# Kernel optimization log

Hardware: AMD Instinct MI355X
Metric: run time of the kernel (lower is better)

The kernel has to match this reference:

```python
import jax, jax.numpy as jnp
import numpy as np
from jax import lax

B = 1024
D_VQ = 64
KS = 1024
KX = 1024
BETA = 0.25


def _conv1d(x, w, b):
    # x: [N, Cin, L], w: [Cout, Cin, 3], 'same' padding
    y = lax.conv_general_dilated(x, w, (1,), [(1, 1)], dimension_numbers=('NCH', 'OIH', 'NCH'))
    return y + b[None, :, None]


def _conv2d(x, w, b):
    # x: [N, Cin, H, W], w: [Cout, Cin, 3, 3], 'same' padding
    y = lax.conv_general_dilated(x, w, (1, 1), [(1, 1), (1, 1)], dimension_numbers=('NCHW', 'OIHW', 'NCHW'))
    return y + b[None, :, None, None]


def _gelu(x):
    return jax.nn.gelu(x, approximate=False)


def _vq_ema(z_e, codebook, beta):
    # z_e: [N, D], codebook: [K, D]
    d = (jnp.sum(z_e * z_e, axis=1, keepdims=True)
         - 2.0 * (z_e @ codebook.T)
         + jnp.sum(codebook * codebook, axis=1)[None, :])  # [N, K]
    idx = jnp.argmin(d, axis=1)                              # [N]
    z_q = codebook[idx]                                      # gather [N, D]
    vq_loss = beta * jnp.mean((z_e - lax.stop_gradient(z_q)) ** 2)
    z_q_st = z_e + lax.stop_gradient(z_q - z_e)              # straight-through
    n = z_e.shape[0]
    probs = jnp.zeros((codebook.shape[0],), z_e.dtype).at[idx].add(1.0) / n
    perplexity = jnp.exp(-jnp.sum(probs * jnp.log(probs + 1e-10)))
    return z_q_st, idx, vq_loss, perplexity


def setup_inputs() -> dict:
    key = jax.random.key(0)
    ks = iter(jax.random.split(key, 40))

    def p(shape, s=0.05):
        return jax.random.normal(next(ks), shape, jnp.float32) * s

    inp = {
        'cubes': jax.random.normal(next(ks), (B, 9, 8, 72), jnp.float32),
        # spectral encoder
        's_w1': p((16, 1, 3)), 's_b1': jnp.zeros((16,), jnp.float32),
        's_w2': p((16, 16, 3)), 's_b2': jnp.zeros((16,), jnp.float32),
        's_fc_w': p((D_VQ, 16 * 8)), 's_fc_b': jnp.zeros((D_VQ,), jnp.float32),
        'cb_s': p((KS, D_VQ), 1.0),
        # spectral decoder
        's_dec_fc_w': p((16 * 8, D_VQ)), 's_dec_fc_b': jnp.zeros((16 * 8,), jnp.float32),
        's_dec_w1': p((16, 16, 3)), 's_dec_b1': jnp.zeros((16,), jnp.float32),
        's_dec_w2': p((1, 16, 3)), 's_dec_b2': jnp.zeros((1,), jnp.float32),
        # spatial encoder
        'x_w1': p((16, 8, 3, 3)), 'x_b1': jnp.zeros((16,), jnp.float32),
        'x_w2': p((16, 16, 3, 3)), 'x_b2': jnp.zeros((16,), jnp.float32),
        'x_fc_w': p((D_VQ, 16 * 3 * 3)), 'x_fc_b': jnp.zeros((D_VQ,), jnp.float32),
        'cb_x': p((KX, D_VQ), 1.0),
        # spatial decoder
        'x_dec_fc_w': p((16 * 3 * 3, D_VQ)), 'x_dec_fc_b': jnp.zeros((16 * 3 * 3,), jnp.float32),
        'x_dec_w1': p((16, 16, 3, 3)), 'x_dec_b1': jnp.zeros((16,), jnp.float32),
        'x_dec_w2': p((8, 16, 3, 3)), 'x_dec_b2': jnp.zeros((8,), jnp.float32),
        'return_recon': 1,
    }
    return inp


def reference(cubes, s_w1, s_b1, s_w2, s_b2, s_fc_w, s_fc_b, cb_s,
              s_dec_fc_w, s_dec_fc_b, s_dec_w1, s_dec_b1, s_dec_w2, s_dec_b2,
              x_w1, x_b1, x_w2, x_b2, x_fc_w, x_fc_b, cb_x,
              x_dec_fc_w, x_dec_fc_b, x_dec_w1, x_dec_b1, x_dec_w2, x_dec_b2,
              return_recon):
    b, p, t, f = cubes.shape
    n = b * p * t
    c6 = cubes.reshape(b, p, t, 8, 3, 3)                   # [B,P,T,8,3,3]
    cperm = jnp.transpose(c6, (0, 1, 2, 4, 5, 3))          # [B,P,T,3,3,8]

    # --- spectral path ---
    spec = jnp.mean(cperm, axis=(3, 4))                    # [B,P,T,8]
    spec_seq = spec.reshape(n, 1, 8)
    s = _gelu(_conv1d(spec_seq, s_w1, s_b1))
    s = _gelu(_conv1d(s, s_w2, s_b2))
    z_e_s = s.reshape(n, 16 * 8) @ s_fc_w.T + s_fc_b       # [N,D]
    z_q_s, k_idx, vq_loss_s, perplex_s = _vq_ema(z_e_s, cb_s, BETA)
    emb_s = z_q_s.reshape(b, p, t, D_VQ)
    k_idx = k_idx.reshape(b, p, t)

    # --- spatial path ---
    spatial = c6.reshape(n, 8, 3, 3)
    x = _gelu(_conv2d(spatial, x_w1, x_b1))
    x = _gelu(_conv2d(x, x_w2, x_b2))
    z_e_x = x.reshape(n, 16 * 9) @ x_fc_w.T + x_fc_b
    z_q_x, m_idx, vq_loss_x, perplex_x = _vq_ema(z_e_x, cb_x, BETA)
    emb_x = z_q_x.reshape(b, p, t, D_VQ)
    m_idx = m_idx.reshape(b, p, t)

    total = vq_loss_s + vq_loss_x

    if return_recon:
        s_dec = (z_q_s @ s_dec_fc_w.T + s_dec_fc_b).reshape(n, 16, 8)
        s_dec = _gelu(_conv1d(s_dec, s_dec_w1, s_dec_b1))
        recon_s = _conv1d(s_dec, s_dec_w2, s_dec_b2)[:, 0, :].reshape(b, p, t, 8)
        recon_loss_s = jnp.mean((recon_s - spec) ** 2)

        x_dec = (z_q_x @ x_dec_fc_w.T + x_dec_fc_b).reshape(n, 16, 3, 3)
        x_dec = _gelu(_conv2d(x_dec, x_dec_w1, x_dec_b1))
        recon_x = _conv2d(x_dec, x_dec_w2, x_dec_b2)        # [N,8,3,3]
        recon_loss_x = jnp.mean((recon_x - spatial) ** 2)
        recon_loss_total = recon_loss_s + recon_loss_x
    else:
        recon_loss_total = jnp.float32(0.0)

    return (emb_s, emb_x, k_idx, m_idx, total, perplex_s, perplex_x, recon_loss_total)
```

## Files before the change

kernel.cpp:

```cpp
#include <hip/hip_runtime.h>
#include <math.h>

#define NTOK 73728

__device__ __forceinline__ float gelu_f(float x) {
    return 0.5f * x * (1.0f + erff(x * 0.70710678118654752440f));
}

__global__ void k_norms(const float* __restrict__ cb_s, const float* __restrict__ cb_x,
                        double* __restrict__ cn_s, double* __restrict__ cn_x) {
    int i = blockIdx.x * blockDim.x + threadIdx.x;
    if (i >= 2048) return;
    const float* cb = (i < 1024) ? cb_s : cb_x;
    double* cn = (i < 1024) ? cn_s : cn_x;
    int c = i & 1023;
    double s = 0.0;
    for (int k = 0; k < 64; ++k) { double v = (double)cb[c * 64 + k]; s += v * v; }
    cn[c] = s;
}

__global__ void k_transpose(const float* __restrict__ src, float* __restrict__ dst, int E) {
    int i = blockIdx.x * 256 + threadIdx.x;
    if (i >= 64 * E) return;
    int e = i >> 6, d = i & 63;
    dst[i] = src[d * E + e];
}

__global__ void k_weff_s(const float* __restrict__ w1, const float* __restrict__ b1,
                         const float* __restrict__ dfcw, const float* __restrict__ dfcb,
                         float* __restrict__ weffT, float* __restrict__ beff) {
    int idx = blockIdx.x * 256 + threadIdx.x;
    if (idx >= 128 * 64) return;
    int o = idx >> 6, d = idx & 63;
    int c = o >> 3, l = o & 7;
    double acc = 0.0;
    for (int ci = 0; ci < 16; ++ci)
        for (int dd = 0; dd < 3; ++dd) {
            int ll = l + dd - 1;
            if (ll < 0 || ll > 7) continue;
            acc += (double)w1[(c * 16 + ci) * 3 + dd] * (double)dfcw[(ci * 8 + ll) * 64 + d];
        }
    weffT[d * 132 + o] = (float)acc;
    if (o < 4) weffT[d * 132 + 128 + o] = 0.f;
    if (d == 0) {
        double bb = (double)b1[c];
        for (int ci = 0; ci < 16; ++ci)
            for (int dd = 0; dd < 3; ++dd) {
                int ll = l + dd - 1;
                if (ll < 0 || ll > 7) continue;
                bb += (double)w1[(c * 16 + ci) * 3 + dd] * (double)dfcb[ci * 8 + ll];
            }
        beff[o] = (float)bb;
    }
}

__global__ void k_weff_x(const float* __restrict__ w1, const float* __restrict__ b1,
                         const float* __restrict__ dfcw, const float* __restrict__ dfcb,
                         float* __restrict__ weffT, float* __restrict__ beff) {
    int idx = blockIdx.x * 256 + threadIdx.x;
    if (idx >= 144 * 64) return;
    int o = idx >> 6, d = idx & 63;
    int c = o / 9, p = o - c * 9;
    int i = p / 3, j = p % 3;
    double acc = 0.0;
    for (int ci = 0; ci < 16; ++ci)
        for (int di = 0; di < 3; ++di) {
            int ii = i + di - 1; if (ii < 0 || ii > 2) continue;
            for (int dj = 0; dj < 3; ++dj) {
                int jj = j + dj - 1; if (jj < 0 || jj > 2) continue;
                acc += (double)w1[((c * 16 + ci) * 3 + di) * 3 + dj]
                     * (double)dfcw[(ci * 9 + ii * 3 + jj) * 64 + d];
            }
        }
    weffT[d * 148 + o] = (float)acc;
    if (o < 4) weffT[d * 148 + 144 + o] = 0.f;
    if (d == 0) {
        double bb = (double)b1[c];
        for (int ci = 0; ci < 16; ++ci)
            for (int di = 0; di < 3; ++di) {
                int ii = i + di - 1; if (ii < 0 || ii > 2) continue;
                for (int dj = 0; dj < 3; ++dj) {
                    int jj = j + dj - 1; if (jj < 0 || jj > 2) continue;
                    bb += (double)w1[((c * 16 + ci) * 3 + di) * 3 + dj]
                        * (double)dfcb[ci * 9 + ii * 3 + jj];
                }
            }
        beff[o] = (float)bb;
    }
}

__global__ void __launch_bounds__(256) k_spec_enc(
    const float* __restrict__ cubes,
    const float* __restrict__ w1, const float* __restrict__ b1,
    const float* __restrict__ w2, const float* __restrict__ b2,
    const float* __restrict__ fcwT, const float* __restrict__ fcb,
    float* __restrict__ z_out)
{
    __shared__ float S[16 * 8];
    __shared__ float A[16 * 136];
    __shared__ float Bb[16 * 136];
    int tid = threadIdx.x;
    int t = tid >> 4, c = tid & 15;
    if (tid < 128) {
        int tk = tid >> 3, f = tid & 7;
        const float* cu = cubes + ((size_t)blockIdx.x * 16 + tk) * 72 + f * 9;
        float s = 0.f;
        #pragma unroll
        for (int k = 0; k < 9; ++k) s += cu[k];
        S[tk * 8 + f] = s * (1.0f / 9.0f);
    }
    __syncthreads();
    {
        float s0[8];
        *(float4*)&s0[0] = *(const float4*)&S[t * 8];
        *(float4*)&s0[4] = *(const float4*)&S[t * 8 + 4];
        float wa = w1[c * 3 + 0], wb = w1[c * 3 + 1], wc = w1[c * 3 + 2], bb = b1[c];
        #pragma unroll
        for (int l = 0; l < 8; ++l) {
            float v = fmaf(wb, s0[l], bb);
            if (l > 0) v = fmaf(wa, s0[l - 1], v);
            if (l < 7) v = fmaf(wc, s0[l + 1], v);
            A[t * 136 + c * 8 + l] = gelu_f(v);
        }
    }
    __syncthreads();
    {
        float acc[8];
        #pragma unroll
        for (int l = 0; l < 8; ++l) acc[l] = b2[c];
        for (int ci = 0; ci < 16; ++ci) {
            float r[8];
            *(float4*)&r[0] = *(const float4*)&A[t * 136 + ci * 8];
            *(float4*)&r[4] = *(const float4*)&A[t * 136 + ci * 8 + 4];
            float wa = w2[(c * 16 + ci) * 3 + 0], wb = w2[(c * 16 + ci) * 3 + 1], wc = w2[(c * 16 + ci) * 3 + 2];
            #pragma unroll
            for (int l = 0; l < 8; ++l) {
                if (l > 0) acc[l] = fmaf(wa, r[l - 1], acc[l]);
                acc[l] = fmaf(wb, r[l], acc[l]);
                if (l < 7) acc[l] = fmaf(wc, r[l + 1], acc[l]);
            }
        }
        #pragma unroll
        for (int l = 0; l < 8; ++l) Bb[t * 136 + c * 8 + l] = gelu_f(acc[l]);
    }
    __syncthreads();
    {
        float4 zv = make_float4(fcb[c * 4 + 0], fcb[c * 4 + 1], fcb[c * 4 + 2], fcb[c * 4 + 3]);
        #pragma unroll 4
        for (int e = 0; e < 128; ++e) {
            float be = Bb[t * 136 + e];
            float4 wv = *(const float4*)(fcwT + (e << 6) + (c << 2));
            zv.x = fmaf(wv.x, be, zv.x);
            zv.y = fmaf(wv.y, be, zv.y);
            zv.z = fmaf(wv.z, be, zv.z);
            zv.w = fmaf(wv.w, be, zv.w);
        }
        *(float4*)(z_out + ((size_t)blockIdx.x * 16 + t) * 64 + c * 4) = zv;
    }
}

__global__ void __launch_bounds__(256) k_spat_enc(
    const float* __restrict__ cubes,
    const float* __restrict__ w1, const float* __restrict__ b1,
    const float* __restrict__ w2, const float* __restrict__ b2,
    const float* __restrict__ fcwT, const float* __restrict__ fcb,
    float* __restrict__ z_out)
{
    __shared__ float A[16 * 200];
    __shared__ float Bb[16 * 200];
    int tid = threadIdx.x;
    int t = tid >> 4, c = tid & 15;
    for (int u = tid; u < 1152; u += 256) {
        int tk = u / 72, e = u - tk * 72;
        int ci = e / 9, p = e - ci * 9;
        A[tk * 200 + ci * 12 + p] = cubes[(size_t)blockIdx.x * 1152 + u];
    }
    __syncthreads();
    {
        float acc[9];
        #pragma unroll
        for (int p = 0; p < 9; ++p) acc[p] = b1[c];
        for (int ci = 0; ci < 8; ++ci) {
            float r[12];
            *(float4*)&r[0] = *(const float4*)&A[t * 200 + ci * 12];
            *(float4*)&r[4] = *(const float4*)&A[t * 200 + ci * 12 + 4];
            *(float4*)&r[8] = *(const float4*)&A[t * 200 + ci * 12 + 8];
            const float* w = w1 + (c * 8 + ci) * 9;
            #pragma unroll
            for (int p = 0; p < 9; ++p) {
                int i = p / 3, j = p % 3;
                #pragma unroll
                for (int di = 0; di < 3; ++di) {
                    int ii = i + di - 1; if (ii < 0 || ii > 2) continue;
                    #pragma unroll
                    for (int dj = 0; dj < 3; ++dj) {
                        int jj = j + dj - 1; if (jj < 0 || jj > 2) continue;
                        acc[p] = fmaf(w[di * 3 + dj], r[ii * 3 + jj], acc[p]);
                    }
                }
            }
        }
        #pragma unroll
        for (int p = 0; p < 9; ++p) Bb[t * 200 + c * 12 + p] = gelu_f(acc[p]);
    }
    __syncthreads();
    {
        float acc[9];
        #pragma unroll
        for (int p = 0; p < 9; ++p) acc[p] = b2[c];
        for (int ci = 0; ci < 16; ++ci) {
            float r[12];
            *(float4*)&r[0] = *(const float4*)&Bb[t * 200 + ci * 12];
            *(float4*)&r[4] = *(const float4*)&Bb[t * 200 + ci * 12 + 4];
            *(float4*)&r[8] = *(const float4*)&Bb[t * 200 + ci * 12 + 8];
            const float* w = w2 + (c * 16 + ci) * 9;
            #pragma unroll
            for (int p = 0; p < 9; ++p) {
                int i = p / 3, j = p % 3;
                #pragma unroll
                for (int di = 0; di < 3; ++di) {
                    int ii = i + di - 1; if (ii < 0 || ii > 2) continue;
                    #pragma unroll
                    for (int dj = 0; dj < 3; ++dj) {
                        int jj = j + dj - 1; if (jj < 0 || jj > 2) continue;
                        acc[p] = fmaf(w[di * 3 + dj], r[ii * 3 + jj], acc[p]);
                    }
                }
            }
        }
        __syncthreads();
        #pragma unroll
        for (int p = 0; p < 9; ++p) A[t * 200 + c * 12 + p] = gelu_f(acc[p]);
    }
    __syncthreads();
    {
        float4 zv = make_float4(fcb[c * 4 + 0], fcb[c * 4 + 1], fcb[c * 4 + 2], fcb[c * 4 + 3]);
        #pragma unroll 4
        for (int e = 0; e < 144; ++e) {
            int ci = e / 9, p = e - ci * 9;
            float be = A[t * 200 + ci * 12 + p];
            float4 wv = *(const float4*)(fcwT + (e << 6) + (c << 2));
            zv.x = fmaf(wv.x, be, zv.x);
            zv.y = fmaf(wv.y, be, zv.y);
            zv.z = fmaf(wv.z, be, zv.z);
            zv.w = fmaf(wv.w, be, zv.w);
        }
        *(float4*)(z_out + ((size_t)blockIdx.x * 16 + t) * 64 + c * 4) = zv;
    }
}

__global__ void __launch_bounds__(256) k_vq(
    float* __restrict__ emb, const float* __restrict__ cb,
    const double* __restrict__ cn,
    float* __restrict__ idx_out, int* __restrict__ hist,
    double* __restrict__ partial)
{
    __shared__ double pbest[4][64];
    __shared__ int pidx[4][64];
    __shared__ int lh[1024];
    int tid = threadIdx.x;
    int w = tid >> 6, l = tid & 63;
    for (int u = tid; u < 1024; u += 256) lh[u] = 0;
    size_t n = (size_t)blockIdx.x * 64 + l;
    float z[64];
    {
        const float4* zp = (const float4*)(emb + n * 64);
        #pragma unroll
        for (int k = 0; k < 16; ++k) *(float4*)&z[k * 4] = zp[k];
    }
    int base = __builtin_amdgcn_readfirstlane(w << 8);
    const float* crb = cb + ((size_t)base << 6);
    const double* cnb = cn + base;
    double best = 1e300; int bi = base;
    for (int cc = 0; cc < 256; ++cc) {
        const float* cr = crb + (cc << 6);
        float d0 = 0.f, d1 = 0.f, d2 = 0.f, d3 = 0.f;
        #pragma unroll
        for (int k = 0; k < 64; k += 4) {
            d0 = fmaf(z[k + 0], cr[k + 0], d0);
            d1 = fmaf(z[k + 1], cr[k + 1], d1);
            d2 = fmaf(z[k + 2], cr[k + 2], d2);
            d3 = fmaf(z[k + 3], cr[k + 3], d3);
        }
        float dot = (d0 + d1) + (d2 + d3);
        double dd = cnb[cc] - 2.0 * (double)dot;
        if (dd < best) { best = dd; bi = base + cc; }
    }
    pbest[w][l] = best; pidx[w][l] = bi;
    __syncthreads();
    if (w == 0) {
        double b = pbest[0][l]; int bj = pidx[0][l];
        #pragma unroll
        for (int q = 1; q < 4; ++q) {
            double d = pbest[q][l];
            if (d < b) { b = d; bj = pidx[q][l]; }
        }
        idx_out[n] = (float)bj;
        float qv[64];
        {
            const float4* cq = (const float4*)(cb + ((size_t)bj << 6));
            #pragma unroll
            for (int k = 0; k < 16; ++k) *(float4*)&qv[k * 4] = cq[k];
        }
        float vs = 0.f;
        #pragma unroll
        for (int k = 0; k < 64; ++k) { float df = z[k] - qv[k]; vs = fmaf(df, df, vs); }
        float4* zo = (float4*)(emb + n * 64);
        #pragma unroll
        for (int k = 0; k < 16; ++k) zo[k] = *(float4*)&qv[k * 4];
        atomicAdd(&lh[bj], 1);
        double s = (double)vs;
        #pragma unroll
        for (int o = 32; o > 0; o >>= 1) s += __shfl_down(s, o);
        if (l == 0) partial[blockIdx.x] = s;
    }
    __syncthreads();
    for (int u = tid; u < 1024; u += 256) if (lh[u] > 0) atomicAdd(&hist[u], lh[u]);
}

__global__ void __launch_bounds__(256) k_spec_dec(
    const float* __restrict__ emb, const float* __restrict__ cubes,
    const float* __restrict__ weffT, const float* __restrict__ beff,
    const float* __restrict__ w2, const float* __restrict__ b2,
    double* __restrict__ partial)
{
    __shared__ float Z[16 * 72];
    __shared__ float Bb[16 * 136];
    __shared__ float S[16 * 8];
    __shared__ double wred[4];
    int tid = threadIdx.x;
    int t = tid >> 4, c = tid & 15;
    {
        int tk = tid >> 4, dq = tid & 15;
        *(float4*)&Z[tk * 72 + dq * 4] =
            *(const float4*)(emb + (size_t)blockIdx.x * 1024 + (size_t)tid * 4);
    }
    if (tid < 128) {
        int tk = tid >> 3, f = tid & 7;
        const float* cu = cubes + ((size_t)blockIdx.x * 16 + tk) * 72 + f * 9;
        float s = 0.f;
        #pragma unroll
        for (int k = 0; k < 9; ++k) s += cu[k];
        S[tk * 8 + f] = s * (1.0f / 9.0f);
    }
    __syncthreads();
    float zr[64];
    #pragma unroll
    for (int k = 0; k < 16; ++k) *(float4*)&zr[k * 4] = *(const float4*)&Z[t * 72 + k * 4];
    {
        float4 a0 = make_float4(0.f, 0.f, 0.f, 0.f);
        float4 a1 = make_float4(0.f, 0.f, 0.f, 0.f);
        #pragma unroll 8
        for (int k = 0; k < 64; ++k) {
            float zk = zr[k];
            float4 w0 = *(const float4*)(weffT + k * 132 + (c << 2));
            float4 w1v = *(const float4*)(weffT + k * 132 + 64 + (c << 2));
            a0.x = fmaf(w0.x, zk, a0.x); a0.y = fmaf(w0.y, zk, a0.y);
            a0.z = fmaf(w0.z, zk, a0.z); a0.w = fmaf(w0.w, zk, a0.w);
            a1.x = fmaf(w1v.x, zk, a1.x); a1.y = fmaf(w1v.y, zk, a1.y);
            a1.z = fmaf(w1v.z, zk, a1.z); a1.w = fmaf(w1v.w, zk, a1.w);
        }
        int o0 = c << 2, o1 = 64 + (c << 2);
        float4 g0 = make_float4(gelu_f(a0.x + beff[o0 + 0]), gelu_f(a0.y + beff[o0 + 1]),
                                gelu_f(a0.z + beff[o0 + 2]), gelu_f(a0.w + beff[o0 + 3]));
        float4 g1 = make_float4(gelu_f(a1.x + beff[o1 + 0]), gelu_f(a1.y + beff[o1 + 1]),
                                gelu_f(a1.z + beff[o1 + 2]), gelu_f(a1.w + beff[o1 + 3]));
        *(float4*)&Bb[t * 136 + o0] = g0;
        *(float4*)&Bb[t * 136 + o1] = g1;
    }
    __syncthreads();
    float acc2 = 0.f;
    {
        int h = c >> 3, pos = c & 7;
        float a = (h == 0) ? b2[0] : 0.f;
        for (int ci = h * 8; ci < h * 8 + 8; ++ci) {
            const float* w = w2 + ci * 3;
            const float* hb = &Bb[t * 136 + ci * 8];
            if (pos > 0) a = fmaf(w[0], hb[pos - 1], a);
            a = fmaf(w[1], hb[pos], a);
            if (pos < 7) a = fmaf(w[2], hb[pos + 1], a);
        }
        a += __shfl_xor(a, 8);
        if (h == 0) { float df = a - S[t * 8 + pos]; acc2 = df * df; }
    }
    double s = (double)acc2;
    #pragma unroll
    for (int o = 32; o > 0; o >>= 1) s += __shfl_down(s, o);
    if ((tid & 63) == 0) wred[tid >> 6] = s;
    __syncthreads();
    if (tid == 0) partial[blockIdx.x] = wred[0] + wred[1] + wred[2] + wred[3];
}

__global__ void __launch_bounds__(256) k_spat_dec(
    const float* __restrict__ emb, const float* __restrict__ cubes,
    const float* __restrict__ weffT, const float* __restrict__ beff,
    const float* __restrict__ w2, const float* __restrict__ b2,
    double* __restrict__ partial)
{
    __shared__ float Z[16 * 72];
    __shared__ float H[16 * 200];
    __shared__ float T[16 * 104];
    __shared__ double wred[4];
    int tid = threadIdx.x;
    int t = tid >> 4, c = tid & 15;
    {
        int tk = tid >> 4, dq = tid & 15;
        *(float4*)&Z[tk * 72 + dq * 4] =
            *(const float4*)(emb + (size_t)blockIdx.x * 1024 + (size_t)tid * 4);
    }
    for (int u = tid; u < 1152; u += 256) {
        int tk = u / 72, e = u - tk * 72;
        int ci = e / 9, p = e - ci * 9;
        T[tk * 104 + ci * 12 + p] = cubes[(size_t)blockIdx.x * 1152 + u];
    }
    __syncthreads();
    float zr[64];
    #pragma unroll
    for (int k = 0; k < 16; ++k) *(float4*)&zr[k * 4] = *(const float4*)&Z[t * 72 + k * 4];
    {
        float4 a0 = make_float4(0.f, 0.f, 0.f, 0.f);
        float4 a1 = make_float4(0.f, 0.f, 0.f, 0.f);
        float4 a2 = make_float4(0.f, 0.f, 0.f, 0.f);
        #pragma unroll 8
        for (int k = 0; k < 64; ++k) {
            float zk = zr[k];
            float4 w0 = *(const float4*)(weffT + k * 148 + (c << 2));
            float4 w1v = *(const float4*)(weffT + k * 148 + 64 + (c << 2));
            float4 w2v = *(const float4*)(weffT + k * 148 + 128 + (c << 2));
            a0.x = fmaf(w0.x, zk, a0.x); a0.y = fmaf(w0.y, zk, a0.y);
            a0.z = fmaf(w0.z, zk, a0.z); a0.w = fmaf(w0.w, zk, a0.w);
            a1.x = fmaf(w1v.x, zk, a1.x); a1.y = fmaf(w1v.y, zk, a1.y);
            a1.z = fmaf(w1v.z, zk, a1.z); a1.w = fmaf(w1v.w, zk, a1.w);
            a2.x = fmaf(w2v.x, zk, a2.x); a2.y = fmaf(w2v.y, zk, a2.y);
            a2.z = fmaf(w2v.z, zk, a2.z); a2.w = fmaf(w2v.w, zk, a2.w);
        }
        float av[12] = {a0.x, a0.y, a0.z, a0.w, a1.x, a1.y, a1.z, a1.w, a2.x, a2.y, a2.z, a2.w};
        #pragma unroll
        for (int q = 0; q < 12; ++q) {
            int o = (c << 2) + ((q >> 2) << 6) + (q & 3);
            int ch = o / 9, p = o - ch * 9;
            H[t * 200 + ch * 12 + p] = gelu_f(av[q] + beff[o]);
        }
    }
    __syncthreads();
    float acc2 = 0.f;
    {
        int co = c >> 1, h = c & 1;
        float accp[9];
        #pragma unroll
        for (int p = 0; p < 9; ++p) accp[p] = (h == 0) ? b2[co] : 0.f;
        for (int ci = h * 8; ci < h * 8 + 8; ++ci) {
            float r[12];
            *(float4*)&r[0] = *(const float4*)&H[t * 200 + ci * 12];
            *(float4*)&r[4] = *(const float4*)&H[t * 200 + ci * 12 + 4];
            *(float4*)&r[8] = *(const float4*)&H[t * 200 + ci * 12 + 8];
            const float* w = w2 + (co * 16 + ci) * 9;
            #pragma unroll
            for (int p = 0; p < 9; ++p) {
                int i = p / 3, j = p % 3;
                #pragma unroll
                for (int di = 0; di < 3; ++di) {
                    int ii = i + di - 1; if (ii < 0 || ii > 2) continue;
                    #pragma unroll
                    for (int dj = 0; dj < 3; ++dj) {
                        int jj = j + dj - 1; if (jj < 0 || jj > 2) continue;
                        accp[p] = fmaf(w[di * 3 + dj], r[ii * 3 + jj], accp[p]);
                    }
                }
            }
        }
        #pragma unroll
        for (int p = 0; p < 9; ++p) {
            float tot = accp[p] + __shfl_xor(accp[p], 1);
            if (h == 0) { float df = tot - T[t * 104 + co * 12 + p]; acc2 = fmaf(df, df, acc2); }
        }
    }
    double s = (double)acc2;
    #pragma unroll
    for (int o = 32; o > 0; o >>= 1) s += __shfl_down(s, o);
    if ((tid & 63) == 0) wred[tid >> 6] = s;
    __syncthreads();
    if (tid == 0) partial[blockIdx.x] = wred[0] + wred[1] + wred[2] + wred[3];
}

__global__ void __launch_bounds__(256) k_final(
    const double* __restrict__ p_vq_s, const double* __restrict__ p_vq_x,
    const double* __restrict__ p_rec_s, const double* __restrict__ p_rec_x,
    const int* __restrict__ hist_s, const int* __restrict__ hist_x,
    const int* __restrict__ rr,
    float* __restrict__ outscal)
{
    __shared__ double wred[4];
    int tid = threadIdx.x;
    auto bred = [&](double v) -> double {
        #pragma unroll
        for (int o = 32; o > 0; o >>= 1) v += __shfl_down(v, o);
        __syncthreads();
        if ((tid & 63) == 0) wred[tid >> 6] = v;
        __syncthreads();
        return wred[0] + wred[1] + wred[2] + wred[3];
    };
    double a;
    a = 0; for (int t = tid; t < 1152; t += 256) a += p_vq_s[t];
    double vq_s = bred(a);
    a = 0; for (int t = tid; t < 1152; t += 256) a += p_vq_x[t];
    double vq_x = bred(a);
    a = 0; for (int t = tid; t < 4608; t += 256) a += p_rec_s[t];
    double rec_s = bred(a);
    a = 0; for (int t = tid; t < 4608; t += 256) a += p_rec_x[t];
    double rec_x = bred(a);
    a = 0;
    for (int t = tid; t < 1024; t += 256) {
        double cnt = (double)hist_s[t];
        if (cnt > 0.0) { double p = cnt / (double)NTOK; a += p * log(p + 1e-10); }
    }
    double ent_s = bred(a);
    a = 0;
    for (int t = tid; t < 1024; t += 256) {
        double cnt = (double)hist_x[t];
        if (cnt > 0.0) { double p = cnt / (double)NTOK; a += p * log(p + 1e-10); }
    }
    double ent_x = bred(a);
    if (tid == 0) {
        double total = 0.25 * (vq_s / 4718592.0 + vq_x / 4718592.0);
        double rec = (rr[0] != 0) ? (rec_s / 589824.0 + rec_x / 5308416.0) : 0.0;
        outscal[0] = (float)total;
        outscal[1] = (float)exp(-ent_s);
        outscal[2] = (float)exp(-ent_x);
        outscal[3] = (float)rec;
    }
}

extern "C" void kernel_launch(void* const* d_in, const int* in_sizes, int n_in,
                              void* d_out, int out_size, void* d_ws, size_t ws_size,
                              hipStream_t stream)
{
    const float* cubes  = (const float*)d_in[0];
    const float* s_w1   = (const float*)d_in[1];
    const float* s_b1   = (const float*)d_in[2];
    const float* s_w2   = (const float*)d_in[3];
    const float* s_b2   = (const float*)d_in[4];
    const float* s_fcw  = (const float*)d_in[5];
    const float* s_fcb  = (const float*)d_in[6];
    const float* cb_s   = (const float*)d_in[7];
    const float* s_dfcw = (const float*)d_in[8];
    const float* s_dfcb = (const float*)d_in[9];
    const float* s_dw1  = (const float*)d_in[10];
    const float* s_db1  = (const float*)d_in[11];
    const float* s_dw2  = (const float*)d_in[12];
    const float* s_db2  = (const float*)d_in[13];
    const float* x_w1   = (const float*)d_in[14];
    const float* x_b1   = (const float*)d_in[15];
    const float* x_w2   = (const float*)d_in[16];
    const float* x_b2   = (const float*)d_in[17];
    const float* x_fcw  = (const float*)d_in[18];
    const float* x_fcb  = (const float*)d_in[19];
    const float* cb_x   = (const float*)d_in[20];
    const float* x_dfcw = (const float*)d_in[21];
    const float* x_dfcb = (const float*)d_in[22];
    const float* x_dw1  = (const float*)d_in[23];
    const float* x_db1  = (const float*)d_in[24];
    const float* x_dw2  = (const float*)d_in[25];
    const float* x_db2  = (const float*)d_in[26];
    const int*   rr     = (const int*)d_in[27];

    float* out   = (float*)d_out;
    float* emb_s = out;
    float* emb_x = out + 4718592;
    float* kidx  = out + 9437184;
    float* midx  = out + 9510912;
    float* scal  = out + 9584640;

    char* ws = (char*)d_ws;
    int*    hist_s  = (int*)(ws + 0);
    int*    hist_x  = (int*)(ws + 4096);
    double* cn_s    = (double*)(ws + 8192);
    double* cn_x    = (double*)(ws + 16384);
    double* p_vq_s  = (double*)(ws + 24576);
    double* p_vq_x  = (double*)(ws + 33792);
    double* p_rec_s = (double*)(ws + 43008);
    double* p_rec_x = (double*)(ws + 79872);
    float*  beff_s  = (float*)(ws + 116736);
    float*  beff_x  = (float*)(ws + 117248);
    float*  weffT_s = (float*)(ws + 117888);
    float*  weffT_x = (float*)(ws + 151680);
    float*  fcwT_s  = (float*)(ws + 189568);
    float*  fcwT_x  = (float*)(ws + 222336);

    hipMemsetAsync(d_ws, 0, 8192, stream);
    k_norms<<<16, 128, 0, stream>>>(cb_s, cb_x, cn_s, cn_x);
    k_weff_s<<<32, 256, 0, stream>>>(s_dw1, s_db1, s_dfcw, s_dfcb, weffT_s, beff_s);
    k_weff_x<<<36, 256, 0, stream>>>(x_dw1, x_db1, x_dfcw, x_dfcb, weffT_x, beff_x);
    k_transpose<<<32, 256, 0, stream>>>(s_fcw, fcwT_s, 128);
    k_transpose<<<36, 256, 0, stream>>>(x_fcw, fcwT_x, 144);
    k_spec_enc<<<4608, 256, 0, stream>>>(cubes, s_w1, s_b1, s_w2, s_b2, fcwT_s, s_fcb, emb_s);
    k_spat_enc<<<4608, 256, 0, stream>>>(cubes, x_w1, x_b1, x_w2, x_b2, fcwT_x, x_fcb, emb_x);
    k_vq<<<1152, 256, 0, stream>>>(emb_s, cb_s, cn_s, kidx, hist_s, p_vq_s);
    k_vq<<<1152, 256, 0, stream>>>(emb_x, cb_x, cn_x, midx, hist_x, p_vq_x);
    k_spec_dec<<<4608, 256, 0, stream>>>(emb_s, cubes, weffT_s, beff_s, s_dw2, s_db2, p_rec_s);
    k_spat_dec<<<4608, 256, 0, stream>>>(emb_x, cubes, weffT_x, beff_x, x_dw2, x_db2, p_rec_x);
    k_final<<<1, 256, 0, stream>>>(p_vq_s, p_vq_x, p_rec_s, p_rec_x, hist_s, hist_x, rr, scal);
}
```

Before: 1.078 ms.

## Merge prep kernels, transpose conv weights, stage VQ codebook tiles in LDS

Combines the five small preprocessing launches into one k_prep kernel. The same kernel also writes channel-minor transposed copies of the conv weights, so the encoder and decoder conv loops make coalesced weight loads. The VQ kernel now stages 32-row codebook tiles per wave in shared memory with float4 reads, instead of each lane reading rows from global memory. It also drops the per-block LDS histogram in favour of direct global atomics, which may add atomic contention on popular codes.

```diff
diff --git a/kernel.cpp b/kernel.cpp
--- a/kernel.cpp
+++ b/kernel.cpp
@@ -7,92 +7,119 @@
     return 0.5f * x * (1.0f + erff(x * 0.70710678118654752440f));
 }
 
-__global__ void k_norms(const float* __restrict__ cb_s, const float* __restrict__ cb_x,
-                        double* __restrict__ cn_s, double* __restrict__ cn_x) {
-    int i = blockIdx.x * blockDim.x + threadIdx.x;
-    if (i >= 2048) return;
-    const float* cb = (i < 1024) ? cb_s : cb_x;
-    double* cn = (i < 1024) ? cn_s : cn_x;
-    int c = i & 1023;
-    double s = 0.0;
-    for (int k = 0; k < 64; ++k) { double v = (double)cb[c * 64 + k]; s += v * v; }
-    cn[c] = s;
-}
-
-__global__ void k_transpose(const float* __restrict__ src, float* __restrict__ dst, int E) {
-    int i = blockIdx.x * 256 + threadIdx.x;
-    if (i >= 64 * E) return;
-    int e = i >> 6, d = i & 63;
-    dst[i] = src[d * E + e];
-}
-
-__global__ void k_weff_s(const float* __restrict__ w1, const float* __restrict__ b1,
-                         const float* __restrict__ dfcw, const float* __restrict__ dfcb,
-                         float* __restrict__ weffT, float* __restrict__ beff) {
-    int idx = blockIdx.x * 256 + threadIdx.x;
-    if (idx >= 128 * 64) return;
-    int o = idx >> 6, d = idx & 63;
-    int c = o >> 3, l = o & 7;
-    double acc = 0.0;
-    for (int ci = 0; ci < 16; ++ci)
-        for (int dd = 0; dd < 3; ++dd) {
-            int ll = l + dd - 1;
-            if (ll < 0 || ll > 7) continue;
-            acc += (double)w1[(c * 16 + ci) * 3 + dd] * (double)dfcw[(ci * 8 + ll) * 64 + d];
-        }
-    weffT[d * 132 + o] = (float)acc;
-    if (o < 4) weffT[d * 132 + 128 + o] = 0.f;
-    if (d == 0) {
-        double bb = (double)b1[c];
+__global__ void __launch_bounds__(256) k_prep(
+    const float* __restrict__ cb_s, const float* __restrict__ cb_x,
+    double* __restrict__ cn_s, double* __restrict__ cn_x,
+    const float* __restrict__ s_dw1, const float* __restrict__ s_db1,
+    const float* __restrict__ s_dfcw, const float* __restrict__ s_dfcb,
+    float* __restrict__ weffT_s, float* __restrict__ beff_s,
+    const float* __restrict__ x_dw1, const float* __restrict__ x_db1,
+    const float* __restrict__ x_dfcw, const float* __restrict__ x_dfcb,
+    float* __restrict__ weffT_x, float* __restrict__ beff_x,
+    const float* __restrict__ s_fcw, float* __restrict__ fcwT_s,
+    const float* __restrict__ x_fcw, float* __restrict__ fcwT_x,
+    const float* __restrict__ s_w2, float* __restrict__ sw2T,
+    const float* __restrict__ x_w1, float* __restrict__ xw1T,
+    const float* __restrict__ x_w2, float* __restrict__ xw2T,
+    const float* __restrict__ x_dw2, float* __restrict__ xdw2T)
+{
+    int bid = blockIdx.x, tid = threadIdx.x;
+    if (bid < 8) {
+        int i = bid * 256 + tid;
+        const float* cb = (i < 1024) ? cb_s : cb_x;
+        double* cn = (i < 1024) ? cn_s : cn_x;
+        int c = i & 1023;
+        double s = 0.0;
+        for (int k = 0; k < 64; ++k) { double v = (double)cb[c * 64 + k]; s += v * v; }
+        cn[c] = s;
+    } else if (bid < 40) {
+        int idx = (bid - 8) * 256 + tid;
+        int o = idx >> 6, d = idx & 63;
+        int c = o >> 3, l = o & 7;
+        double acc = 0.0;
         for (int ci = 0; ci < 16; ++ci)
             for (int dd = 0; dd < 3; ++dd) {
                 int ll = l + dd - 1;
                 if (ll < 0 || ll > 7) continue;
-                bb += (double)w1[(c * 16 + ci) * 3 + dd] * (double)dfcb[ci * 8 + ll];
+                acc += (double)s_dw1[(c * 16 + ci) * 3 + dd] * (double)s_dfcw[(ci * 8 + ll) * 64 + d];
             }
-        beff[o] = (float)bb;
-    }
-}
-
-__global__ void k_weff_x(const float* __restrict__ w1, const float* __restrict__ b1,
-                         const float* __restrict__ dfcw, const float* __restrict__ dfcb,
-                         float* __restrict__ weffT, float* __restrict__ beff) {
-    int idx = blockIdx.x * 256 + threadIdx.x;
-    if (idx >= 144 * 64) return;
-    int o = idx >> 6, d = idx & 63;
-    int c = o / 9, p = o - c * 9;
-    int i = p / 3, j = p % 3;
-    double acc = 0.0;
-    for (int ci = 0; ci < 16; ++ci)
-        for (int di = 0; di < 3; ++di) {
-            int ii = i + di - 1; if (ii < 0 || ii > 2) continue;
-            for (int dj = 0; dj < 3; ++dj) {
-                int jj = j + dj - 1; if (jj < 0 || jj > 2) continue;
-                acc += (double)w1[((c * 16 + ci) * 3 + di) * 3 + dj]
-                     * (double)dfcw[(ci * 9 + ii * 3 + jj) * 64 + d];
-            }
-        }
-    weffT[d * 148 + o] = (float)acc;
-    if (o < 4) weffT[d * 148 + 144 + o] = 0.f;
-    if (d == 0) {
-        double bb = (double)b1[c];
+        weffT_s[d * 132 + o] = (float)acc;
+        if (o < 4) weffT_s[d * 132 + 128 + o] = 0.f;
+        if (d == 0) {
+            double bb = (double)s_db1[c];
+            for (int ci = 0; ci < 16; ++ci)
+                for (int dd = 0; dd < 3; ++dd) {
+                    int ll = l + dd - 1;
+                    if (ll < 0 || ll > 7) continue;
+                    bb += (double)s_dw1[(c * 16 + ci) * 3 + dd] * (double)s_dfcb[ci * 8 + ll];
+                }
+            beff_s[o] = (float)bb;
+        }
+    } else if (bid < 76) {
+        int idx = (bid - 40) * 256 + tid;
+        int o = idx >> 6, d = idx & 63;
+        int c = o / 9, p = o - c * 9;
+        int i = p / 3, j = p % 3;
+        double acc = 0.0;
         for (int ci = 0; ci < 16; ++ci)
             for (int di = 0; di < 3; ++di) {
                 int ii = i + di - 1; if (ii < 0 || ii > 2) continue;
                 for (int dj = 0; dj < 3; ++dj) {
                     int jj = j + dj - 1; if (jj < 0 || jj > 2) continue;
-                    bb += (double)w1[((c * 16 + ci) * 3 + di) * 3 + dj]
-                        * (double)dfcb[ci * 9 + ii * 3 + jj];
+                    acc += (double)x_dw1[((c * 16 + ci) * 3 + di) * 3 + dj]
+                         * (double)x_dfcw[(ci * 9 + ii * 3 + jj) * 64 + d];
                 }
             }
-        beff[o] = (float)bb;
+        weffT_x[d * 148 + o] = (float)acc;
+        if (o < 4) weffT_x[d * 148 + 144 + o] = 0.f;
+        if (d == 0) {
+            double bb = (double)x_db1[c];
+            for (int ci = 0; ci < 16; ++ci)
+                for (int di = 0; di < 3; ++di) {
+                    int ii = i + di - 1; if (ii < 0 || ii > 2) continue;
+                    for (int dj = 0; dj < 3; ++dj) {
+                        int jj = j + dj - 1; if (jj < 0 || jj > 2) continue;
+                        bb += (double)x_dw1[((c * 16 + ci) * 3 + di) * 3 + dj]
+                            * (double)x_dfcb[ci * 9 + ii * 3 + jj];
+                    }
+                }
+            beff_x[o] = (float)bb;
+        }
+    } else if (bid < 108) {
+        int i = (bid - 76) * 256 + tid;
+        fcwT_s[i] = s_fcw[(i & 63) * 128 + (i >> 6)];
+    } else if (bid < 144) {
+        int i = (bid - 108) * 256 + tid;
+        fcwT_x[i] = x_fcw[(i & 63) * 144 + (i >> 6)];
+    } else {
+        int i = (bid - 144) * 256 + tid;
+        if (i < 768) {
+            int c = i & 15, r = i >> 4;
+            int ci = r / 3, dd = r % 3;
+            sw2T[i] = s_w2[(c * 16 + ci) * 3 + dd];
+        } else if (i < 1920) {
+            int j = i - 768;
+            int c = j & 15, r = j >> 4;
+            int ci = r / 9, tap = r % 9;
+            xw1T[j] = x_w1[(c * 8 + ci) * 9 + tap];
+        } else if (i < 4224) {
+            int j = i - 1920;
+            int c = j & 15, r = j >> 4;
+            int ci = r / 9, tap = r % 9;
+            xw2T[j] = x_w2[(c * 16 + ci) * 9 + tap];
+        } else {
+            int j = i - 4224;
+            int co = j & 7, r = j >> 3;
+            int ci = r / 9, tap = r % 9;
+            xdw2T[j] = x_dw2[(co * 16 + ci) * 9 + tap];
+        }
     }
 }
 
 __global__ void __launch_bounds__(256) k_spec_enc(
     const float* __restrict__ cubes,
     const float* __restrict__ w1, const float* __restrict__ b1,
-    const float* __restrict__ w2, const float* __restrict__ b2,
+    const float* __restrict__ sw2T, const float* __restrict__ b2,
     const float* __restrict__ fcwT, const float* __restrict__ fcb,
     float* __restrict__ z_out)
 {
@@ -132,7 +159,9 @@
             float r[8];
             *(float4*)&r[0] = *(const float4*)&A[t * 136 + ci * 8];
             *(float4*)&r[4] = *(const float4*)&A[t * 136 + ci * 8 + 4];
-            float wa = w2[(c * 16 + ci) * 3 + 0], wb = w2[(c * 16 + ci) * 3 + 1], wc = w2[(c * 16 + ci) * 3 + 2];
+            float wa = sw2T[(ci * 3 + 0) * 16 + c];
+            float wb = sw2T[(ci * 3 + 1) * 16 + c];
+            float wc = sw2T[(ci * 3 + 2) * 16 + c];
             #pragma unroll
             for (int l = 0; l < 8; ++l) {
                 if (l > 0) acc[l] = fmaf(wa, r[l - 1], acc[l]);
@@ -161,8 +190,8 @@
 
 __global__ void __launch_bounds__(256) k_spat_enc(
     const float* __restrict__ cubes,
-    const float* __restrict__ w1, const float* __restrict__ b1,
-    const float* __restrict__ w2, const float* __restrict__ b2,
+    const float* __restrict__ xw1T, const float* __restrict__ b1,
+    const float* __restrict__ xw2T, const float* __restrict__ b2,
     const float* __restrict__ fcwT, const float* __restrict__ fcb,
     float* __restrict__ z_out)
 {
@@ -185,7 +214,9 @@
             *(float4*)&r[0] = *(const float4*)&A[t * 200 + ci * 12];
             *(float4*)&r[4] = *(const float4*)&A[t * 200 + ci * 12 + 4];
             *(float4*)&r[8] = *(const float4*)&A[t * 200 + ci * 12 + 8];
-            const float* w = w1 + (c * 8 + ci) * 9;
+            float wv[9];
+            #pragma unroll
+            for (int q = 0; q < 9; ++q) wv[q] = xw1T[(ci * 9 + q) * 16 + c];
             #pragma unroll
             for (int p = 0; p < 9; ++p) {
                 int i = p / 3, j = p % 3;
@@ -195,7 +226,7 @@
                     #pragma unroll
                     for (int dj = 0; dj < 3; ++dj) {
                         int jj = j + dj - 1; if (jj < 0 || jj > 2) continue;
-                        acc[p] = fmaf(w[di * 3 + dj], r[ii * 3 + jj], acc[p]);
+                        acc[p] = fmaf(wv[di * 3 + dj], r[ii * 3 + jj], acc[p]);
                     }
                 }
             }
@@ -213,7 +244,9 @@
             *(float4*)&r[0] = *(const float4*)&Bb[t * 200 + ci * 12];
             *(float4*)&r[4] = *(const float4*)&Bb[t * 200 + ci * 12 + 4];
             *(float4*)&r[8] = *(const float4*)&Bb[t * 200 + ci * 12 + 8];
-            const float* w = w2 + (c * 16 + ci) * 9;
+            float wv[9];
+            #pragma unroll
+            for (int q = 0; q < 9; ++q) wv[q] = xw2T[(ci * 9 + q) * 16 + c];
             #pragma unroll
             for (int p = 0; p < 9; ++p) {
                 int i = p / 3, j = p % 3;
@@ -223,7 +256,7 @@
                     #pragma unroll
                     for (int dj = 0; dj < 3; ++dj) {
                         int jj = j + dj - 1; if (jj < 0 || jj > 2) continue;
-                        acc[p] = fmaf(w[di * 3 + dj], r[ii * 3 + jj], acc[p]);
+                        acc[p] = fmaf(wv[di * 3 + dj], r[ii * 3 + jj], acc[p]);
                     }
                 }
             }
@@ -255,12 +288,12 @@
     float* __restrict__ idx_out, int* __restrict__ hist,
     double* __restrict__ partial)
 {
+    __shared__ float CB[4][32][68];
+    __shared__ double CNt[4][32];
     __shared__ double pbest[4][64];
     __shared__ int pidx[4][64];
-    __shared__ int lh[1024];
     int tid = threadIdx.x;
     int w = tid >> 6, l = tid & 63;
-    for (int u = tid; u < 1024; u += 256) lh[u] = 0;
     size_t n = (size_t)blockIdx.x * 64 + l;
     float z[64];
     {
@@ -268,23 +301,35 @@
         #pragma unroll
         for (int k = 0; k < 16; ++k) *(float4*)&z[k * 4] = zp[k];
     }
-    int base = __builtin_amdgcn_readfirstlane(w << 8);
-    const float* crb = cb + ((size_t)base << 6);
-    const double* cnb = cn + base;
-    double best = 1e300; int bi = base;
-    for (int cc = 0; cc < 256; ++cc) {
-        const float* cr = crb + (cc << 6);
-        float d0 = 0.f, d1 = 0.f, d2 = 0.f, d3 = 0.f;
-        #pragma unroll
-        for (int k = 0; k < 64; k += 4) {
-            d0 = fmaf(z[k + 0], cr[k + 0], d0);
-            d1 = fmaf(z[k + 1], cr[k + 1], d1);
-            d2 = fmaf(z[k + 2], cr[k + 2], d2);
-            d3 = fmaf(z[k + 3], cr[k + 3], d3);
-        }
-        float dot = (d0 + d1) + (d2 + d3);
-        double dd = cnb[cc] - 2.0 * (double)dot;
-        if (dd < best) { best = dd; bi = base + cc; }
+    double best = 1e300; int bi = w * 256;
+    for (int r = 0; r < 8; ++r) {
+        __syncthreads();
+        #pragma unroll
+        for (int pass = 0; pass < 8; ++pass) {
+            int f = pass * 256 + tid;
+            int ww = f >> 9, cc = (f >> 4) & 31, ch = f & 15;
+            float4 v = *(const float4*)(cb + ((size_t)(ww * 256 + r * 32 + cc) << 6) + (ch << 2));
+            *(float4*)&CB[ww][cc][ch << 2] = v;
+        }
+        if (tid < 128) CNt[tid >> 5][tid & 31] = cn[(tid >> 5) * 256 + r * 32 + (tid & 31)];
+        __syncthreads();
+        int base = w * 256 + r * 32;
+        #pragma unroll 4
+        for (int cc = 0; cc < 32; ++cc) {
+            const float* cr = &CB[w][cc][0];
+            float d0 = 0.f, d1 = 0.f, d2 = 0.f, d3 = 0.f;
+            #pragma unroll
+            for (int k = 0; k < 64; k += 4) {
+                float4 v = *(const float4*)(cr + k);
+                d0 = fmaf(z[k + 0], v.x, d0);
+                d1 = fmaf(z[k + 1], v.y, d1);
+                d2 = fmaf(z[k + 2], v.z, d2);
+                d3 = fmaf(z[k + 3], v.w, d3);
+            }
+            float dot = (d0 + d1) + (d2 + d3);
+            double dd = CNt[w][cc] - 2.0 * (double)dot;
+            if (dd < best) { best = dd; bi = base + cc; }
+        }
     }
     pbest[w][l] = best; pidx[w][l] = bi;
     __syncthreads();
@@ -308,14 +353,12 @@
         float4* zo = (float4*)(emb + n * 64);
         #pragma unroll
         for (int k = 0; k < 16; ++k) zo[k] = *(float4*)&qv[k * 4];
-        atomicAdd(&lh[bj], 1);
+        atomicAdd(&hist[bj], 1);
         double s = (double)vs;
         #pragma unroll
         for (int o = 32; o > 0; o >>= 1) s += __shfl_down(s, o);
         if (l == 0) partial[blockIdx.x] = s;
     }
-    __syncthreads();
-    for (int u = tid; u < 1024; u += 256) if (lh[u] > 0) atomicAdd(&hist[u], lh[u]);
 }
 
 __global__ void __launch_bounds__(256) k_spec_dec(
@@ -394,7 +437,7 @@
 __global__ void __launch_bounds__(256) k_spat_dec(
     const float* __restrict__ emb, const float* __restrict__ cubes,
     const float* __restrict__ weffT, const float* __restrict__ beff,
-    const float* __restrict__ w2, const float* __restrict__ b2,
+    const float* __restrict__ xdw2T, const float* __restrict__ b2,
     double* __restrict__ partial)
 {
     __shared__ float Z[16 * 72];
@@ -454,7 +497,9 @@
             *(float4*)&r[0] = *(const float4*)&H[t * 200 + ci * 12];
             *(float4*)&r[4] = *(const float4*)&H[t * 200 + ci * 12 + 4];
             *(float4*)&r[8] = *(const float4*)&H[t * 200 + ci * 12 + 8];
-            const float* w = w2 + (co * 16 + ci) * 9;
+            float wv[9];
+            #pragma unroll
+            for (int q = 0; q < 9; ++q) wv[q] = xdw2T[(ci * 9 + q) * 8 + co];
             #pragma unroll
             for (int p = 0; p < 9; ++p) {
                 int i = p / 3, j = p % 3;
@@ -464,7 +509,7 @@
                     #pragma unroll
                     for (int dj = 0; dj < 3; ++dj) {
                         int jj = j + dj - 1; if (jj < 0 || jj > 2) continue;
-                        accp[p] = fmaf(w[di * 3 + dj], r[ii * 3 + jj], accp[p]);
+                        accp[p] = fmaf(wv[di * 3 + dj], r[ii * 3 + jj], accp[p]);
                     }
                 }
             }
@@ -582,22 +627,26 @@
     double* p_rec_x = (double*)(ws + 79872);
     float*  beff_s  = (float*)(ws + 116736);
     float*  beff_x  = (float*)(ws + 117248);
-    float*  weffT_s = (float*)(ws + 117888);
-    float*  weffT_x = (float*)(ws + 151680);
-    float*  fcwT_s  = (float*)(ws + 189568);
-    float*  fcwT_x  = (float*)(ws + 222336);
+    float*  weffT_s = (float*)(ws + 117824);
+    float*  weffT_x = (float*)(ws + 151616);
+    float*  fcwT_s  = (float*)(ws + 189504);
+    float*  fcwT_x  = (float*)(ws + 222272);
+    float*  sw2T    = (float*)(ws + 259136);
+    float*  xw1T    = (float*)(ws + 262208);
+    float*  xw2T    = (float*)(ws + 266816);
+    float*  xdw2T   = (float*)(ws + 276032);
 
     hipMemsetAsync(d_ws, 0, 8192, stream);
-    k_norms<<<16, 128, 0, stream>>>(cb_s, cb_x, cn_s, cn_x);
-    k_weff_s<<<32, 256, 0, stream>>>(s_dw1, s_db1, s_dfcw, s_dfcb, weffT_s, beff_s);
-    k_weff_x<<<36, 256, 0, stream>>>(x_dw1, x_db1, x_dfcw, x_dfcb, weffT_x, beff_x);
-    k_transpose<<<32, 256, 0, stream>>>(s_fcw, fcwT_s, 128);
-    k_transpose<<<36, 256, 0, stream>>>(x_fcw, fcwT_x, 144);
-    k_spec_enc<<<4608, 256, 0, stream>>>(cubes, s_w1, s_b1, s_w2, s_b2, fcwT_s, s_fcb, emb_s);
-    k_spat_enc<<<4608, 256, 0, stream>>>(cubes, x_w1, x_b1, x_w2, x_b2, fcwT_x, x_fcb, emb_x);
+    k_prep<<<165, 256, 0, stream>>>(cb_s, cb_x, cn_s, cn_x,
+                                    s_dw1, s_db1, s_dfcw, s_dfcb, weffT_s, beff_s,
+                                    x_dw1, x_db1, x_dfcw, x_dfcb, weffT_x, beff_x,
+                                    s_fcw, fcwT_s, x_fcw, fcwT_x,
+                                    s_w2, sw2T, x_w1, xw1T, x_w2, xw2T, x_dw2, xdw2T);
+    k_spec_enc<<<4608, 256, 0, stream>>>(cubes, s_w1, s_b1, sw2T, s_b2, fcwT_s, s_fcb, emb_s);
+    k_spat_enc<<<4608, 256, 0, stream>>>(cubes, xw1T, x_b1, xw2T, x_b2, fcwT_x, x_fcb, emb_x);
     k_vq<<<1152, 256, 0, stream>>>(emb_s, cb_s, cn_s, kidx, hist_s, p_vq_s);
     k_vq<<<1152, 256, 0, stream>>>(emb_x, cb_x, cn_x, midx, hist_x, p_vq_x);
     k_spec_dec<<<4608, 256, 0, stream>>>(emb_s, cubes, weffT_s, beff_s, s_dw2, s_db2, p_rec_s);
-    k_spat_dec<<<4608, 256, 0, stream>>>(emb_x, cubes, weffT_x, beff_x, x_dw2, x_db2, p_rec_x);
+    k_spat_dec<<<4608, 256, 0, stream>>>(emb_x, cubes, weffT_x, beff_x, xdw2T, x_db2, p_rec_x);
     k_final<<<1, 256, 0, stream>>>(p_vq_s, p_vq_x, p_rec_s, p_rec_x, hist_s, hist_x, rr, scal);
 }
```

After: 2.396 ms. 2.22x slower.
